# Optimization experiments

Hardware: AMD Instinct MI355X
Metric: run time of the kernel (lower is better)

Reference implementation:

```python
import jax, jax.numpy as jnp
import numpy as np

B, S, H, E, V = 64, 1024, 1024, 1024, 50257


def setup_inputs() -> dict:
    key = jax.random.key(0)
    ks = jax.random.split(key, 12)
    x = jax.random.randint(ks[0], (B, 1), 0, V, dtype=jnp.int64)
    h = jax.random.normal(ks[1], (B, H), dtype=jnp.float32)
    c = jax.random.normal(ks[2], (B, H), dtype=jnp.float32)
    encoder_output = jax.random.normal(ks[3], (B, S, H), dtype=jnp.float32)
    length = jax.random.randint(ks[4], (B,), 1, S + 1, dtype=jnp.int32)
    length = length.at[0].set(S)  # mask width is length[0]; must equal S
    scale = 0.02
    emb = jax.random.normal(ks[5], (V, E), dtype=jnp.float32) * scale
    W_ih = jax.random.normal(ks[6], (4 * H, E), dtype=jnp.float32) * scale
    b_ih = jnp.zeros((4 * H,), dtype=jnp.float32)
    W_hh = jax.random.normal(ks[7], (4 * H, H), dtype=jnp.float32) * scale
    b_hh = jnp.zeros((4 * H,), dtype=jnp.float32)
    W_bilin = jax.random.normal(ks[8], (H, H), dtype=jnp.float32) * scale
    W_out = jax.random.normal(ks[9], (V, 2 * H), dtype=jnp.float32) * scale
    b_out = jnp.zeros((V,), dtype=jnp.float32)
    return {"x": x, "h": h, "c": c, "encoder_output": encoder_output,
            "length": length, "emb": emb, "W_ih": W_ih, "b_ih": b_ih,
            "W_hh": W_hh, "b_hh": b_hh, "W_bilin": W_bilin,
            "W_out": W_out, "b_out": b_out}


def reference(x, h, c, encoder_output, length, emb, W_ih, b_ih, W_hh, b_hh,
              W_bilin, W_out, b_out):
    # embedding + squeeze(1); dropout is identity in eval mode
    xe = emb[x[:, 0]]  # [B, E]
    # LSTMCell: gates in PyTorch order i, f, g, o
    gates = xe @ W_ih.T + b_ih + h @ W_hh.T + b_hh  # [B, 4H]
    i_g, f_g, g_g, o_g = jnp.split(gates, 4, axis=-1)
    i_g = jax.nn.sigmoid(i_g)
    f_g = jax.nn.sigmoid(f_g)
    g_g = jnp.tanh(g_g)
    o_g = jax.nn.sigmoid(o_g)
    c_new = f_g * c + i_g * g_g
    h_new = o_g * jnp.tanh(c_new)  # [B, H]
    # bilinear attention energy: (h W) . enc
    energy = jnp.einsum('bh,hk,bsk->bs', h_new, W_bilin, encoder_output)
    # mask multiplies energy BEFORE softmax (faithful to original code)
    mask = (jnp.arange(S)[None, :] < length[:, None]).astype(energy.dtype)
    attn = jax.nn.softmax(energy * mask, axis=-1)  # [B, S]
    context = jnp.einsum('bs,bsh->bh', attn, encoder_output)  # [B, H]
    output = jnp.concatenate([context, h_new], axis=1) @ W_out.T + b_out  # [B, V]
    return output, h_new, c_new
```

## Files before the change

kernel.cpp:

```cpp
#include <hip/hip_runtime.h>
#include <math.h>

constexpr int NB = 64;
constexpr int NS = 1024;
constexpr int NH = 1024;
constexpr int NE = 1024;
constexpr int NV = 50257;
constexpr int NK2 = 2048;

typedef __bf16 bf16_8 __attribute__((ext_vector_type(8)));
typedef float  f32x4  __attribute__((ext_vector_type(4)));

__device__ inline f32x4 ntload4(const float* p) {
  return __builtin_nontemporal_load((const f32x4*)p);
}

__global__ __launch_bounds__(256) void k_cvtAg(const int* __restrict__ x,
    const float* __restrict__ h, const float* __restrict__ emb,
    __bf16* __restrict__ Ag) {
  int t = blockIdx.x * 256 + threadIdx.x;
  int b = t >> 11, k = t & 2047;
  float v = (k < NE) ? emb[(size_t)x[b] * NE + k] : h[b * NH + (k - NE)];
  Ag[t] = (__bf16)v;
}

__global__ __launch_bounds__(256) void k_gates_mfma(const __bf16* __restrict__ Ag,
    const float* __restrict__ Wih, const float* __restrict__ bih,
    const float* __restrict__ Whh, const float* __restrict__ bhh,
    float* __restrict__ gates) {
  __shared__ f32x4 red[4][4][64];
  int lane = threadIdx.x & 63;
  int wave = threadIdx.x >> 6;
  int col  = lane & 15;
  int grp  = lane >> 4;
  int j    = blockIdx.x * 16 + col;

  const float* Wsel = (wave < 2) ? Wih : Whh;
  const float*  wp  = Wsel + (size_t)j * 1024 + (wave & 1) * 512 + grp * 8;
  const __bf16* ap  = Ag + wave * 512 + grp * 8;

  f32x4 acc[4] = {};
#pragma unroll 4
  for (int ks = 0; ks < 16; ++ks) {
    int kb = ks * 32;
    f32x4 b0 = ntload4(wp + kb);
    f32x4 b1 = ntload4(wp + kb + 4);
    bf16_8 bf;
    bf[0] = (__bf16)b0[0]; bf[1] = (__bf16)b0[1];
    bf[2] = (__bf16)b0[2]; bf[3] = (__bf16)b0[3];
    bf[4] = (__bf16)b1[0]; bf[5] = (__bf16)b1[1];
    bf[6] = (__bf16)b1[2]; bf[7] = (__bf16)b1[3];
#pragma unroll
    for (int m = 0; m < 4; ++m) {
      bf16_8 a = *(const bf16_8*)(ap + (m * 16 + col) * NK2 + kb);
      acc[m] = __builtin_amdgcn_mfma_f32_16x16x32_bf16(a, bf, acc[m], 0, 0, 0);
    }
  }
#pragma unroll
  for (int m = 0; m < 4; ++m) red[wave][m][lane] = acc[m];
  __syncthreads();
  f32x4 s = red[0][wave][lane];
#pragma unroll
  for (int wv = 1; wv < 4; ++wv) s += red[wv][wave][lane];
  float bias = bih[j] + bhh[j];
  int b = wave * 16 + grp * 4;
#pragma unroll
  for (int r = 0; r < 4; ++r)
    gates[(b + r) * 4096 + j] = s[r] + bias;
}

__global__ __launch_bounds__(256) void k_lstm(const float* __restrict__ gates,
    const float* __restrict__ c, float* __restrict__ hc_out,
    __bf16* __restrict__ A_bf) {
  int t = blockIdx.x * 256 + threadIdx.x;
  int b = t >> 10, hh = t & 1023;
  float ig = gates[b * 4096 + hh];
  float fg = gates[b * 4096 + 1024 + hh];
  float gg = gates[b * 4096 + 2048 + hh];
  float og = gates[b * 4096 + 3072 + hh];
  float i_ = 1.f / (1.f + expf(-ig));
  float f_ = 1.f / (1.f + expf(-fg));
  float g_ = tanhf(gg);
  float o_ = 1.f / (1.f + expf(-og));
  float cn = f_ * c[t] + i_ * g_;
  float hn = o_ * tanhf(cn);
  hc_out[t] = hn;
  hc_out[NB * NH + t] = cn;
  A_bf[b * NK2 + 1024 + hh] = (__bf16)hn;
}

__global__ __launch_bounds__(256) void k_bilin(const float* __restrict__ hnew,
    const float* __restrict__ Wb, float* __restrict__ t_out) {
  int b = blockIdx.x >> 2;
  int k = ((blockIdx.x & 3) << 8) + threadIdx.x;
  const float* hb = hnew + b * NH;
  float acc = 0.f;
#pragma unroll 8
  for (int hh = 0; hh < NH; ++hh)
    acc += hb[hh] * Wb[hh * NH + k];
  t_out[b * NH + k] = acc;
}

__global__ __launch_bounds__(256) void k_attn(const float* __restrict__ t_in,
    const float* __restrict__ enc, const int* __restrict__ length,
    float* __restrict__ ctxp, float* __restrict__ ml) {
  int b     = blockIdx.x >> 4;
  int strip = ((blockIdx.x & 15) << 2) + (threadIdx.x >> 6);
  int lane  = threadIdx.x & 63;
  int len   = length[b];
  int s0    = strip * 16;

  const float* tp = t_in + b * NH;
  f32x4 tv[4];
#pragma unroll
  for (int i = 0; i < 4; ++i) tv[i] = *(const f32x4*)(tp + (i * 64 + lane) * 4);

  const float* ep = enc + ((size_t)b * NS + s0) * NH;

  float m_run = -1e30f, l_run = 0.f;
  f32x4 acc[4] = {};

#pragma unroll 2
  for (int r = 0; r < 16; ++r) {
    f32x4 e[4];
#pragma unroll
    for (int i = 0; i < 4; ++i) e[i] = ntload4(ep + (r * 256 + i * 64 + lane) * 4);
    float d = 0.f;
#pragma unroll
    for (int i = 0; i < 4; ++i)
      d += tv[i][0] * e[i][0] + tv[i][1] * e[i][1] + tv[i][2] * e[i][2] + tv[i][3] * e[i][3];
#pragma unroll
    for (int off = 32; off; off >>= 1) d += __shfl_xor(d, off);
    float v = (s0 + r < len) ? d : 0.f;
    float m_new = fmaxf(m_run, v);
    float f = expf(m_run - m_new);
    float w = expf(v - m_new);
    l_run = l_run * f + w;
#pragma unroll
    for (int i = 0; i < 4; ++i)
      acc[i] = acc[i] * f + w * e[i];
    m_run = m_new;
  }

  int idx = b * 64 + strip;
  float* P = ctxp + (size_t)idx * 1024;
#pragma unroll
  for (int i = 0; i < 4; ++i)
    *(f32x4*)(P + (i * 64 + lane) * 4) = acc[i];
  if (lane == 0) {
    ml[idx * 2]     = m_run;
    ml[idx * 2 + 1] = l_run;
  }
}

__global__ __launch_bounds__(256) void k_attn_combine(const float* __restrict__ ctxp,
    const float* __restrict__ ml, __bf16* __restrict__ A_bf) {
  int b = blockIdx.x;
  int tid = threadIdx.x;
  float M = -1e30f;
#pragma unroll
  for (int c = 0; c < 64; ++c) M = fmaxf(M, ml[(b * 64 + c) * 2]);
  float Z = 0.f;
  f32x4 num = {0.f, 0.f, 0.f, 0.f};
#pragma unroll 4
  for (int c = 0; c < 64; ++c) {
    float e = expf(ml[(b * 64 + c) * 2] - M);
    Z += e * ml[(b * 64 + c) * 2 + 1];
    f32x4 p = *(const f32x4*)(ctxp + ((size_t)(b * 64 + c)) * 1024 + tid * 4);
    num += e * p;
  }
  float inv = 1.f / Z;
  __bf16* dst = A_bf + b * NK2 + tid * 4;
#pragma unroll
  for (int i = 0; i < 4; ++i) dst[i] = (__bf16)(num[i] * inv);
}

__global__ __launch_bounds__(64) void k_out_mfma(const __bf16* __restrict__ A,
    const float* __restrict__ Wout, const float* __restrict__ bout,
    float* __restrict__ out) {
  int lane = threadIdx.x;
  int col  = lane & 15;
  int grp  = lane >> 4;
  int vb   = blockIdx.x * 32;
  int va   = vb + col;
  int vc   = vb + 16 + col;
  int vaC  = va < NV ? va : NV - 1;
  int vcC  = vc < NV ? vc : NV - 1;

  const float*  wpA = Wout + (size_t)vaC * NK2 + grp * 8;
  const float*  wpB = Wout + (size_t)vcC * NK2 + grp * 8;
  const __bf16* ap  = A + grp * 8;

  f32x4 acc[4][2] = {};

#pragma unroll 2
  for (int ks = 0; ks < 64; ++ks) {
    int kb = ks * 32;
    f32x4 a0 = ntload4(wpA + kb);
    f32x4 a1 = ntload4(wpA + kb + 4);
    f32x4 c0 = ntload4(wpB + kb);
    f32x4 c1 = ntload4(wpB + kb + 4);
    bf16_8 bfA, bfB;
    bfA[0] = (__bf16)a0[0]; bfA[1] = (__bf16)a0[1];
    bfA[2] = (__bf16)a0[2]; bfA[3] = (__bf16)a0[3];
    bfA[4] = (__bf16)a1[0]; bfA[5] = (__bf16)a1[1];
    bfA[6] = (__bf16)a1[2]; bfA[7] = (__bf16)a1[3];
    bfB[0] = (__bf16)c0[0]; bfB[1] = (__bf16)c0[1];
    bfB[2] = (__bf16)c0[2]; bfB[3] = (__bf16)c0[3];
    bfB[4] = (__bf16)c1[0]; bfB[5] = (__bf16)c1[1];
    bfB[6] = (__bf16)c1[2]; bfB[7] = (__bf16)c1[3];
#pragma unroll
    for (int m = 0; m < 4; ++m) {
      bf16_8 a = *(const bf16_8*)(ap + (size_t)(m * 16 + col) * NK2 + kb);
      acc[m][0] = __builtin_amdgcn_mfma_f32_16x16x32_bf16(a, bfA, acc[m][0], 0, 0, 0);
      acc[m][1] = __builtin_amdgcn_mfma_f32_16x16x32_bf16(a, bfB, acc[m][1], 0, 0, 0);
    }
  }

#pragma unroll
  for (int n = 0; n < 2; ++n) {
    int vrow = vb + n * 16 + col;
    if (vrow < NV) {
      float bb = bout[vrow];
      int mrow = grp * 4;
#pragma unroll
      for (int m = 0; m < 4; ++m)
#pragma unroll
        for (int r = 0; r < 4; ++r)
          out[(size_t)(m * 16 + mrow + r) * NV + vrow] = acc[m][n][r] + bb;
    }
  }
}

extern "C" void kernel_launch(void* const* d_in, const int* in_sizes, int n_in,
                              void* d_out, int out_size, void* d_ws, size_t ws_size,
                              hipStream_t stream) {
  const int*   x      = (const int*)d_in[0];
  const float* h      = (const float*)d_in[1];
  const float* c      = (const float*)d_in[2];
  const float* enc    = (const float*)d_in[3];
  const int*   length = (const int*)d_in[4];
  const float* emb    = (const float*)d_in[5];
  const float* Wih    = (const float*)d_in[6];
  const float* bih    = (const float*)d_in[7];
  const float* Whh    = (const float*)d_in[8];
  const float* bhh    = (const float*)d_in[9];
  const float* Wb     = (const float*)d_in[10];
  const float* Wout   = (const float*)d_in[11];
  const float* bout   = (const float*)d_in[12];

  float* out = (float*)d_out;
  float* hn  = out + (size_t)NB * NV;

  float* ws      = (float*)d_ws;
  float* gates   = ws;
  float* t_ws    = gates + NB * 4 * NH;
  float* ctxp    = t_ws + NB * NH;
  float* ml      = ctxp + 64 * (size_t)NB * 1024;
  __bf16* A_bf   = (__bf16*)(ml + NB * 128);
  __bf16* Ag_bf  = A_bf + NB * NK2;

  k_cvtAg<<<NB * NK2 / 256, 256, 0, stream>>>(x, h, emb, Ag_bf);
  k_gates_mfma<<<4096 / 16, 256, 0, stream>>>(Ag_bf, Wih, bih, Whh, bhh, gates);
  k_lstm<<<NB * NH / 256, 256, 0, stream>>>(gates, c, hn, A_bf);
  k_bilin<<<NB * 4, 256, 0, stream>>>(hn, Wb, t_ws);
  k_attn<<<NB * 16, 256, 0, stream>>>(t_ws, enc, length, ctxp, ml);
  k_attn_combine<<<NB, 256, 0, stream>>>(ctxp, ml, A_bf);
  k_out_mfma<<<(NV + 31) / 32, 64, 0, stream>>>(A_bf, Wout, bout, out);
}
```

Before: 269.7 us.

## Fuse embedding gather into gates GEMM, raise unroll, nontemporal output stores

Measured after the change: 307.2 us. +13.9%, slower.

```diff
diff --git a/kernel.cpp b/kernel.cpp
--- a/kernel.cpp
+++ b/kernel.cpp
@@ -15,16 +15,8 @@
   return __builtin_nontemporal_load((const f32x4*)p);
 }
 
-__global__ __launch_bounds__(256) void k_cvtAg(const int* __restrict__ x,
+__global__ __launch_bounds__(256) void k_gates_mfma(const int* __restrict__ x,
     const float* __restrict__ h, const float* __restrict__ emb,
-    __bf16* __restrict__ Ag) {
-  int t = blockIdx.x * 256 + threadIdx.x;
-  int b = t >> 11, k = t & 2047;
-  float v = (k < NE) ? emb[(size_t)x[b] * NE + k] : h[b * NH + (k - NE)];
-  Ag[t] = (__bf16)v;
-}
-
-__global__ __launch_bounds__(256) void k_gates_mfma(const __bf16* __restrict__ Ag,
     const float* __restrict__ Wih, const float* __restrict__ bih,
     const float* __restrict__ Whh, const float* __restrict__ bhh,
     float* __restrict__ gates) {
@@ -37,7 +29,14 @@
 
   const float* Wsel = (wave < 2) ? Wih : Whh;
   const float*  wp  = Wsel + (size_t)j * 1024 + (wave & 1) * 512 + grp * 8;
-  const __bf16* ap  = Ag + wave * 512 + grp * 8;
+
+  const float* asrc[4];
+#pragma unroll
+  for (int m = 0; m < 4; ++m) {
+    int row = m * 16 + col;
+    if (wave < 2) asrc[m] = emb + (size_t)x[row] * NE + (wave & 1) * 512 + grp * 8;
+    else          asrc[m] = h + row * NH + (wave & 1) * 512 + grp * 8;
+  }
 
   f32x4 acc[4] = {};
 #pragma unroll 4
@@ -52,8 +51,14 @@
     bf[6] = (__bf16)b1[2]; bf[7] = (__bf16)b1[3];
 #pragma unroll
     for (int m = 0; m < 4; ++m) {
-      bf16_8 a = *(const bf16_8*)(ap + (m * 16 + col) * NK2 + kb);
-      acc[m] = __builtin_amdgcn_mfma_f32_16x16x32_bf16(a, bf, acc[m], 0, 0, 0);
+      f32x4 a0 = *(const f32x4*)(asrc[m] + kb);
+      f32x4 a1 = *(const f32x4*)(asrc[m] + kb + 4);
+      bf16_8 af;
+      af[0] = (__bf16)a0[0]; af[1] = (__bf16)a0[1];
+      af[2] = (__bf16)a0[2]; af[3] = (__bf16)a0[3];
+      af[4] = (__bf16)a1[0]; af[5] = (__bf16)a1[1];
+      af[6] = (__bf16)a1[2]; af[7] = (__bf16)a1[3];
+      acc[m] = __builtin_amdgcn_mfma_f32_16x16x32_bf16(af, bf, acc[m], 0, 0, 0);
     }
   }
 #pragma unroll
@@ -120,7 +125,7 @@
   float m_run = -1e30f, l_run = 0.f;
   f32x4 acc[4] = {};
 
-#pragma unroll 2
+#pragma unroll 4
   for (int r = 0; r < 16; ++r) {
     f32x4 e[4];
 #pragma unroll
@@ -193,7 +198,7 @@
 
   f32x4 acc[4][2] = {};
 
-#pragma unroll 2
+#pragma unroll 4
   for (int ks = 0; ks < 64; ++ks) {
     int kb = ks * 32;
     f32x4 a0 = ntload4(wpA + kb);
@@ -227,7 +232,8 @@
       for (int m = 0; m < 4; ++m)
 #pragma unroll
         for (int r = 0; r < 4; ++r)
-          out[(size_t)(m * 16 + mrow + r) * NV + vrow] = acc[m][n][r] + bb;
+          __builtin_nontemporal_store(acc[m][n][r] + bb,
+              out + (size_t)(m * 16 + mrow + r) * NV + vrow);
     }
   }
 }
@@ -258,10 +264,8 @@
   float* ctxp    = t_ws + NB * NH;
   float* ml      = ctxp + 64 * (size_t)NB * 1024;
   __bf16* A_bf   = (__bf16*)(ml + NB * 128);
-  __bf16* Ag_bf  = A_bf + NB * NK2;
-
-  k_cvtAg<<<NB * NK2 / 256, 256, 0, stream>>>(x, h, emb, Ag_bf);
-  k_gates_mfma<<<4096 / 16, 256, 0, stream>>>(Ag_bf, Wih, bih, Whh, bhh, gates);
+
+  k_gates_mfma<<<4096 / 16, 256, 0, stream>>>(x, h, emb, Wih, bih, Whh, bhh, gates);
   k_lstm<<<NB * NH / 256, 256, 0, stream>>>(gates, c, hn, A_bf);
   k_bilin<<<NB * 4, 256, 0, stream>>>(hn, Wb, t_ws);
   k_attn<<<NB * 16, 256, 0, stream>>>(t_ws, enc, length, ctxp, ml);
```
